# Kernel optimization log

Hardware: AMD Instinct MI355X
Metric: run time of the kernel (lower is better)

The kernel has to match this reference:

```python
import jax, jax.numpy as jnp
import numpy as np

N_GROUP = 64
GROUP_SIZE = 64
INPUT_DIM = 2048
BATCH = 8192
N_MONTN = 512


def setup_inputs() -> dict:
    key = jax.random.key(0)
    k1, k2, k3, k4, k5 = jax.random.split(key, 5)
    x = jax.random.normal(k1, (BATCH, INPUT_DIM), dtype=jnp.float32)
    weight = jax.random.normal(k2, (N_GROUP * GROUP_SIZE, INPUT_DIM), dtype=jnp.float32) * 0.02
    bias = jax.random.normal(k3, (N_GROUP * GROUP_SIZE,), dtype=jnp.float32) * 0.02
    rand_u = jax.random.uniform(k4, (BATCH,), dtype=jnp.float32)
    montn_index = jax.random.randint(k5, (N_MONTN,), 0, INPUT_DIM, dtype=jnp.int32)
    return {"x": x, "weight": weight, "bias": bias, "rand_u": rand_u,
            "montn_index": montn_index}


def reference(x, weight, bias, rand_u, montn_index):
    # Square the weights on monotone input columns (in-place in torch).
    w = weight.at[:, montn_index].set(weight[:, montn_index] ** 2)
    # y = x @ w^T + b  -> [B, n_group * n_group_size]
    y = jnp.einsum('bi,oi->bo', x, w) + bias
    B = y.shape[0]
    # per-group min over contiguous slices, then max over groups
    group_mins = y.reshape(B, N_GROUP, GROUP_SIZE).min(axis=2)  # [B, n_group]
    out = group_mins.max(axis=1)                                 # [B]
    # vectorized Bernoulli: 1.0 if u < sigmoid(out) else 0.0
    sample = (rand_u < jax.nn.sigmoid(out)).astype(jnp.float32)
    return sample.reshape(-1, 1)
```

## Files before the change

### kernel.cpp

```cpp
#include <hip/hip_runtime.h>
#include <cmath>


typedef _Float16 f16x8 __attribute__((ext_vector_type(8)));
typedef float f32x4 __attribute__((ext_vector_type(4)));

#define MARGIN_EPS 4e-3f
#define MAX_UNDEC 96

__device__ __forceinline__ void async_load16(const void* gptr, void* lptr) {
  __builtin_amdgcn_global_load_lds(
      (const __attribute__((address_space(1))) void*)gptr,
      (__attribute__((address_space(3))) void*)lptr, 16, 0, 0);
}

__device__ __forceinline__ float us2f(unsigned short u) {
  return (float)__builtin_bit_cast(_Float16, u);
}

__device__ __forceinline__ unsigned f2key(float f) {
  unsigned b = __float_as_uint(f);
  return (b & 0x80000000u) ? ~b : (b | 0x80000000u);
}
__device__ __forceinline__ float key2f(unsigned e) {
  unsigned b = (e & 0x80000000u) ? (e ^ 0x80000000u) : ~e;
  return __uint_as_float(b);
}


__global__ void convert_hi(const float* __restrict__ x,
                           const float* __restrict__ wgt,
                           unsigned short* __restrict__ xo,
                           unsigned short* __restrict__ wo,
                           const int* __restrict__ montn,
                           int* __restrict__ count) {
  __shared__ unsigned msk[64];
  const int b = blockIdx.x, t = threadIdx.x;
  const int l = t & 63, w = t >> 6;
  const int r = b * 4 + w;
  const int use_mask = (r >= 8192) ? 1 : 0;
  if (b == 0 && t == 0) *count = 0;
  if (use_mask) {
    if (t < 64) msk[t] = 0u;
    __syncthreads();
    for (int j = t; j < 512; j += 256) {
      const int c = montn[j];
      atomicOr(&msk[c >> 5], 1u << (c & 31));
    }
    __syncthreads();
  }
  const float* rowp = use_mask ? (wgt + (size_t)(r - 8192) * 2048)
                               : (x + (size_t)r * 2048);
  unsigned short* up = use_mask ? (wo + (size_t)(r - 8192) * 2048)
                                : (xo + (size_t)r * 2048);
  float4 v[4][2];
#pragma unroll
  for (int p = 0; p < 4; ++p) {
    v[p][0] = ((const float4*)rowp)[p * 128 + 2 * l];
    v[p][1] = ((const float4*)rowp)[p * 128 + 2 * l + 1];
  }
  unsigned mw[4];
#pragma unroll
  for (int p = 0; p < 4; ++p)
    mw[p] = use_mask ? msk[p * 16 + (l >> 2)] : 0u;

#pragma unroll
  for (int p = 0; p < 4; ++p) {
    float f[8];
    f[0] = v[p][0].x; f[1] = v[p][0].y; f[2] = v[p][0].z; f[3] = v[p][0].w;
    f[4] = v[p][1].x; f[5] = v[p][1].y; f[6] = v[p][1].z; f[7] = v[p][1].w;
    unsigned short hs[8];
#pragma unroll
    for (int c = 0; c < 8; ++c) {
      float g = f[c];
      if ((mw[p] >> (8 * (l & 3) + c)) & 1u) g = g * g;
      hs[c] = __builtin_bit_cast(unsigned short, (_Float16)g);
    }
    uint4 H;
    H.x = (unsigned)hs[0] | ((unsigned)hs[1] << 16);
    H.y = (unsigned)hs[2] | ((unsigned)hs[3] << 16);
    H.z = (unsigned)hs[4] | ((unsigned)hs[5] << 16);
    H.w = (unsigned)hs[6] | ((unsigned)hs[7] << 16);
    *((uint4*)(up + p * 512 + 8 * l)) = H;
  }
}

__global__ __launch_bounds__(256, 2) void gemm_minmax(
    const unsigned short* __restrict__ X, const unsigned short* __restrict__ W,
    const float* __restrict__ bias, float* __restrict__ pmax) {
  __shared__ unsigned short As[128 * 64];
  __shared__ unsigned short Bs[256 * 64];
  const int t = threadIdx.x;
  const int lane = t & 63;
  const int w = t >> 6;
  const int wm = w >> 1, wn = w & 1;
  const int lin = blockIdx.x;
  const int sid = lin >> 3;
  const int m0 = (sid >> 1) * 128;
  const int nb = (lin & 7) * 2 + (sid & 1);
  const int n0 = nb * 256;

  const int rowBase = w * 8 + (lane >> 3);
  const int gchunk = ((lane & 7) ^ ((lane >> 3) & 7)) * 8;
  const size_t gA0 = (size_t)(m0 + rowBase) * 2048 + gchunk;
  const size_t gB0 = (size_t)(n0 + rowBase) * 2048 + gchunk;
  unsigned short* ldsA0 = As + w * 512;
  unsigned short* ldsB0 = Bs + w * 512;

  const int am = lane & 15, quad = lane >> 4;
  int arow[4], brow[8];
#pragma unroll
  for (int i = 0; i < 4; ++i) arow[i] = (wm * 64 + i * 16 + am) * 64;
#pragma unroll
  for (int j = 0; j < 8; ++j) brow[j] = (wn * 128 + j * 16 + am) * 64;
  int swz[2];
#pragma unroll
  for (int h = 0; h < 2; ++h) swz[h] = (((h << 2) + quad) ^ (am & 7)) * 8;

  f32x4 acc[4][8];
#pragma unroll
  for (int i = 0; i < 4; ++i)
#pragma unroll
    for (int j = 0; j < 8; ++j) acc[i][j] = (f32x4){0.f, 0.f, 0.f, 0.f};

#pragma unroll 1
  for (int it = 0; it < 32; ++it) {
    const int kin = it * 64;
    __syncthreads();
#pragma unroll
    for (int c = 0; c < 4; ++c)
      async_load16(X + gA0 + (size_t)(c * 32) * 2048 + kin, ldsA0 + c * 2048);
#pragma unroll
    for (int c = 0; c < 8; ++c)
      async_load16(W + gB0 + (size_t)(c * 32) * 2048 + kin, ldsB0 + c * 2048);
    __syncthreads();

#pragma unroll
    for (int h = 0; h < 2; ++h) {
      f16x8 av[4], bv[8];
#pragma unroll
      for (int i = 0; i < 4; ++i) av[i] = *(const f16x8*)(As + arow[i] + swz[h]);
#pragma unroll
      for (int j = 0; j < 8; ++j) bv[j] = *(const f16x8*)(Bs + brow[j] + swz[h]);
#pragma unroll
      for (int mb = 0; mb < 4; ++mb)
#pragma unroll
        for (int nb8 = 0; nb8 < 8; ++nb8)
          acc[mb][nb8] = __builtin_amdgcn_mfma_f32_16x16x32_f16(
              av[mb], bv[nb8], acc[mb][nb8], 0, 0, 0);
    }
  }

  float bv8[8];
#pragma unroll
  for (int nb8 = 0; nb8 < 8; ++nb8)
    bv8[nb8] = bias[n0 + wn * 128 + nb8 * 16 + am];
  float vml[4][4];
#pragma unroll
  for (int mb = 0; mb < 4; ++mb) {
#pragma unroll
    for (int reg = 0; reg < 4; ++reg) {
      float vm = -3.4e38f;
#pragma unroll
      for (int hh = 0; hh < 2; ++hh) {
        float v = fminf(
            fminf(acc[mb][4 * hh + 0][reg] + bv8[4 * hh + 0],
                  acc[mb][4 * hh + 1][reg] + bv8[4 * hh + 1]),
            fminf(acc[mb][4 * hh + 2][reg] + bv8[4 * hh + 2],
                  acc[mb][4 * hh + 3][reg] + bv8[4 * hh + 3]));
        v = fminf(v, __shfl_xor(v, 1, 64));
        v = fminf(v, __shfl_xor(v, 2, 64));
        v = fminf(v, __shfl_xor(v, 4, 64));
        v = fminf(v, __shfl_xor(v, 8, 64));
        vm = fmaxf(vm, v);
      }
      vml[mb][reg] = vm;
    }
  }
  __syncthreads();
  float* pbuf = (float*)As;
  if (wn == 1 && am == 0) {
#pragma unroll
    for (int mb = 0; mb < 4; ++mb)
#pragma unroll
      for (int reg = 0; reg < 4; ++reg)
        pbuf[wm * 64 + mb * 16 + quad * 4 + reg] = vml[mb][reg];
  }
  __syncthreads();
  if (wn == 0 && am == 0) {
#pragma unroll
    for (int mb = 0; mb < 4; ++mb)
#pragma unroll
      for (int reg = 0; reg < 4; ++reg) {
        const int ridx = wm * 64 + mb * 16 + quad * 4 + reg;
        pmax[(size_t)(m0 + ridx) * 16 + nb] = fmaxf(vml[mb][reg], pbuf[ridx]);
      }
  }
}

__global__ void finalize_margin(const float* __restrict__ pmax,
                                const float* __restrict__ rand_u,
                                float* __restrict__ out,
                                int* __restrict__ count,
                                int* __restrict__ undec) {
  const int row = blockIdx.x * 256 + threadIdx.x;
  const float4* pp = (const float4*)(pmax + (size_t)row * 16);
  const float4 a = pp[0], b4 = pp[1], c4 = pp[2], d4 = pp[3];
  float v = fmaxf(fmaxf(fmaxf(a.x, a.y), fmaxf(a.z, a.w)),
                  fmaxf(fmaxf(b4.x, b4.y), fmaxf(b4.z, b4.w)));
  v = fmaxf(v, fmaxf(fmaxf(c4.x, c4.y), fmaxf(c4.z, c4.w)));
  v = fmaxf(v, fmaxf(fmaxf(d4.x, d4.y), fmaxf(d4.z, d4.w)));
  const float u = rand_u[row];
  const float slo = 1.0f / (1.0f + expf(-(v - MARGIN_EPS)));
  const float shi = 1.0f / (1.0f + expf(-(v + MARGIN_EPS)));
  if (u < slo) {
    out[row] = 1.0f;
  } else if (u >= shi) {
    out[row] = 0.0f;
  } else {
    const int i = atomicAdd(count, 1);
    if (i < 8192) undec[i] = row;
  }
}

__global__ __launch_bounds__(256) void recompute_fp32(
    const float* __restrict__ X, const float* __restrict__ W,
    const int* __restrict__ montn, const int* __restrict__ count,
    const int* __restrict__ undec, float* __restrict__ ypart) {
  __shared__ float wf[64 * 129];
  __shared__ float part[256];
  __shared__ unsigned msk[64];
  const int g = blockIdx.x, kc = blockIdx.y;
  const int t = threadIdx.x;
  int n = *count;
  if (n > MAX_UNDEC) n = MAX_UNDEC;
  if (n == 0) return;

  if (t < 64) msk[t] = 0u;
  __syncthreads();
  for (int j = t; j < 512; j += 256) {
    const int c = montn[j];
    atomicOr(&msk[c >> 5], 1u << (c & 31));
  }
  __syncthreads();

  {
    const int cl = t >> 2, ks = t & 3;
    const int k0 = kc * 128 + ks * 32;
    const float* wp = W + (size_t)(g * 64 + cl) * 2048 + k0;
    float* dst = wf + cl * 129 + ks * 32;
    const unsigned mword = msk[k0 >> 5];
#pragma unroll
    for (int i = 0; i < 32; i += 4) {
      float4 wv = *(const float4*)(wp + i);
      float f0 = wv.x, f1 = wv.y, f2 = wv.z, f3 = wv.w;
      if ((mword >> (i + 0)) & 1u) f0 *= f0;
      if ((mword >> (i + 1)) & 1u) f1 *= f1;
      if ((mword >> (i + 2)) & 1u) f2 *= f2;
      if ((mword >> (i + 3)) & 1u) f3 *= f3;
      dst[i + 0] = f0; dst[i + 1] = f1; dst[i + 2] = f2; dst[i + 3] = f3;
    }
  }
  __syncthreads();

  const int col = t & 63, kq = t >> 6;
  const float* wcol = wf + col * 129 + kq * 32;
  float* yout = ypart + (size_t)kc * (96 * 4096);
  for (int s = 0; s < n; ++s) {
    const int row = undec[s];
    const float* xp = X + (size_t)row * 2048 + kc * 128 + kq * 32;
    float acc = 0.f;
#pragma unroll
    for (int i = 0; i < 32; i += 4) {
      float4 xv = *(const float4*)(xp + i);
      acc = fmaf(xv.x, wcol[i + 0], acc);
      acc = fmaf(xv.y, wcol[i + 1], acc);
      acc = fmaf(xv.z, wcol[i + 2], acc);
      acc = fmaf(xv.w, wcol[i + 3], acc);
    }
    part[t] = acc;
    __syncthreads();
    if (t < 64) {
      const float yv = part[t] + part[t + 64] + part[t + 128] + part[t + 192];
      yout[(size_t)s * 4096 + g * 64 + t] = yv;
    }
    __syncthreads();
  }
}

__global__ void decide(const float* __restrict__ ypart,
                       const int* __restrict__ undec,
                       const int* __restrict__ count,
                       const float* __restrict__ bias,
                       const float* __restrict__ rand_u,
                       float* __restrict__ out) {
  __shared__ float gm[64];
  int n = *count;
  if (n > MAX_UNDEC) n = MAX_UNDEC;
  const int s = blockIdx.x;
  if (s >= n) return;
  const int t = threadIdx.x, w = t >> 6;
  const float* yb = ypart + (size_t)s * 4096;
#pragma unroll 1
  for (int e = 0; e < 16; ++e) {
    const int c = t + e * 256;
    float y = bias[c];
#pragma unroll
    for (int kc = 0; kc < 16; ++kc)
      y += yb[(size_t)kc * (96 * 4096) + c];
    y = fminf(y, __shfl_xor(y, 1, 64));
    y = fminf(y, __shfl_xor(y, 2, 64));
    y = fminf(y, __shfl_xor(y, 4, 64));
    y = fminf(y, __shfl_xor(y, 8, 64));
    y = fminf(y, __shfl_xor(y, 16, 64));
    y = fminf(y, __shfl_xor(y, 32, 64));
    if ((t & 63) == 0) gm[w + 4 * e] = y;
  }
  __syncthreads();
  if (t < 64) {
    float v = gm[t];
    v = fmaxf(v, __shfl_xor(v, 1, 64));
    v = fmaxf(v, __shfl_xor(v, 2, 64));
    v = fmaxf(v, __shfl_xor(v, 4, 64));
    v = fmaxf(v, __shfl_xor(v, 8, 64));
    v = fmaxf(v, __shfl_xor(v, 16, 64));
    v = fmaxf(v, __shfl_xor(v, 32, 64));
    if (t == 0) {
      const int row = undec[s];
      const float sg = 1.0f / (1.0f + expf(-v));
      out[row] = (rand_u[row] < sg) ? 1.0f : 0.0f;
    }
  }
}

__global__ void convert_split_fb(float* __restrict__ x, float* __restrict__ wgt,
                                 const int* __restrict__ montn,
                                 int* __restrict__ count,
                                 unsigned* __restrict__ gmax) {
  const int b = blockIdx.x;
  const int t = threadIdx.x;
  if (b >= 3072) {
    gmax[(b - 3072) * 256 + t] = 0u;
    return;
  }
  __shared__ unsigned msk[64];
  const int l = t & 63, w = t >> 6;
  const int r = b * 4 + w;
  const int use_mask = (r >= 8192) ? 1 : 0;
  if (b == 0 && t == 0) *count = 0;
  if (use_mask) {
    if (t < 64) msk[t] = 0u;
    __syncthreads();
    for (int j = t; j < 512; j += 256) {
      const int c = montn[j];
      atomicOr(&msk[c >> 5], 1u << (c & 31));
    }
    __syncthreads();
  }
  float* rowp = use_mask ? (wgt + (size_t)(r - 8192) * 2048)
                         : (x + (size_t)r * 2048);
  float4 v[4][2];
#pragma unroll
  for (int p = 0; p < 4; ++p) {
    v[p][0] = ((const float4*)rowp)[p * 128 + 2 * l];
    v[p][1] = ((const float4*)rowp)[p * 128 + 2 * l + 1];
  }
  unsigned mw[4];
#pragma unroll
  for (int p = 0; p < 4; ++p)
    mw[p] = use_mask ? msk[p * 16 + (l >> 2)] : 0u;

  unsigned short* up = (unsigned short*)rowp;
#pragma unroll
  for (int p = 0; p < 4; ++p) {
    float f[8];
    f[0] = v[p][0].x; f[1] = v[p][0].y; f[2] = v[p][0].z; f[3] = v[p][0].w;
    f[4] = v[p][1].x; f[5] = v[p][1].y; f[6] = v[p][1].z; f[7] = v[p][1].w;
    unsigned short hs[8], ls[8];
#pragma unroll
    for (int c = 0; c < 8; ++c) {
      float g = f[c];
      if ((mw[p] >> (8 * (l & 3) + c)) & 1u) g = g * g;
      _Float16 h = (_Float16)g;
      float res = g - (float)h;
      _Float16 lo = (_Float16)res;
      hs[c] = __builtin_bit_cast(unsigned short, h);
      ls[c] = __builtin_bit_cast(unsigned short, lo);
    }
    uint4 H, L;
    H.x = (unsigned)hs[0] | ((unsigned)hs[1] << 16);
    H.y = (unsigned)hs[2] | ((unsigned)hs[3] << 16);
    H.z = (unsigned)hs[4] | ((unsigned)hs[5] << 16);
    H.w = (unsigned)hs[6] | ((unsigned)hs[7] << 16);
    L.x = (unsigned)ls[0] | ((unsigned)ls[1] << 16);
    L.y = (unsigned)ls[2] | ((unsigned)ls[3] << 16);
    L.z = (unsigned)ls[4] | ((unsigned)ls[5] << 16);
    L.w = (unsigned)ls[6] | ((unsigned)ls[7] << 16);
    *((uint4*)(up + p * 512 + 8 * l)) = H;
    *((uint4*)(up + 2048 + p * 512 + 8 * l)) = L;
  }
}

__global__ __launch_bounds__(256, 2) void gemm_minmax_fb(
    const unsigned short* __restrict__ X, const unsigned short* __restrict__ W,
    const float* __restrict__ bias, unsigned* __restrict__ gmax) {
  __shared__ unsigned short As[128 * 64];
  __shared__ unsigned short Bs[256 * 64];
  const int t = threadIdx.x;
  const int lane = t & 63;
  const int w = t >> 6;
  const int wm = w >> 1, wn = w & 1;
  const int lin = blockIdx.x;
  const int sid = lin >> 3;
  const int m0 = (sid >> 1) * 128;
  const int n0 = ((lin & 7) * 2 + (sid & 1)) * 256;

  const int rowBase = w * 8 + (lane >> 3);
  const int gchunk = ((lane & 7) ^ ((lane >> 3) & 7)) * 8;
  const size_t gA0 = (size_t)(m0 + rowBase) * 4096 + gchunk;
  const size_t gB0 = (size_t)(n0 + rowBase) * 4096 + gchunk;
  unsigned short* ldsA0 = As + w * 512;
  unsigned short* ldsB0 = Bs + w * 512;

  const int am = lane & 15, quad = lane >> 4;
  int arow[4], brow[8];
#pragma unroll
  for (int i = 0; i < 4; ++i) arow[i] = (wm * 64 + i * 16 + am) * 64;
#pragma unroll
  for (int j = 0; j < 8; ++j) brow[j] = (wn * 128 + j * 16 + am) * 64;
  int swz[2];
#pragma unroll
  for (int h = 0; h < 2; ++h) swz[h] = (((h << 2) + quad) ^ (am & 7)) * 8;

  f32x4 acc[4][8];
#pragma unroll
  for (int i = 0; i < 4; ++i)
#pragma unroll
    for (int j = 0; j < 8; ++j) acc[i][j] = (f32x4){0.f, 0.f, 0.f, 0.f};

#pragma unroll 1
  for (int it = 0; it < 32; ++it) {
    const int kin = it * 64;
    __syncthreads();
#pragma unroll
    for (int c = 0; c < 4; ++c)
      async_load16(X + gA0 + (size_t)(c * 32) * 4096 + kin, ldsA0 + c * 2048);
#pragma unroll
    for (int c = 0; c < 8; ++c)
      async_load16(W + gB0 + (size_t)(c * 32) * 4096 + kin, ldsB0 + c * 2048);
    __syncthreads();

#pragma unroll
    for (int h = 0; h < 2; ++h) {
      f16x8 av[4], bv[8];
#pragma unroll
      for (int i = 0; i < 4; ++i) av[i] = *(const f16x8*)(As + arow[i] + swz[h]);
#pragma unroll
      for (int j = 0; j < 8; ++j) bv[j] = *(const f16x8*)(Bs + brow[j] + swz[h]);
#pragma unroll
      for (int mb = 0; mb < 4; ++mb)
#pragma unroll
        for (int nb = 0; nb < 8; ++nb)
          acc[mb][nb] = __builtin_amdgcn_mfma_f32_16x16x32_f16(
              av[mb], bv[nb], acc[mb][nb], 0, 0, 0);
    }
  }

  float bv8[8];
#pragma unroll
  for (int nb = 0; nb < 8; ++nb) bv8[nb] = bias[n0 + wn * 128 + nb * 16 + am];
#pragma unroll
  for (int mb = 0; mb < 4; ++mb) {
#pragma unroll
    for (int reg = 0; reg < 4; ++reg) {
      float vm = -3.4e38f;
#pragma unroll
      for (int hh = 0; hh < 2; ++hh) {
        float v = fminf(
            fminf(acc[mb][4 * hh + 0][reg] + bv8[4 * hh + 0],
                  acc[mb][4 * hh + 1][reg] + bv8[4 * hh + 1]),
            fminf(acc[mb][4 * hh + 2][reg] + bv8[4 * hh + 2],
                  acc[mb][4 * hh + 3][reg] + bv8[4 * hh + 3]));
        v = fminf(v, __shfl_xor(v, 1, 64));
        v = fminf(v, __shfl_xor(v, 2, 64));
        v = fminf(v, __shfl_xor(v, 4, 64));
        v = fminf(v, __shfl_xor(v, 8, 64));
        vm = fmaxf(vm, v);
      }
      if (am == 0) {
        const int row = m0 + wm * 64 + mb * 16 + quad * 4 + reg;
        atomicMax(&gmax[row], f2key(vm));
      }
    }
  }
}

__global__ void finalize_margin_fb(const unsigned* __restrict__ gmax,
                                   const float* __restrict__ rand_u,
                                   float* __restrict__ out,
                                   int* __restrict__ count,
                                   int* __restrict__ undec,
                                   float4* __restrict__ ybuf4) {
  const int t = threadIdx.x;
  ybuf4[(size_t)blockIdx.x * 256 + t] = (float4){0.f, 0.f, 0.f, 0.f};
  if (blockIdx.x < 32) {
    const int row = blockIdx.x * 256 + t;
    const float v = key2f(gmax[row]);
    const float u = rand_u[row];
    const float slo = 1.0f / (1.0f + expf(-(v - MARGIN_EPS)));
    const float shi = 1.0f / (1.0f + expf(-(v + MARGIN_EPS)));
    if (u < slo) {
      out[row] = 1.0f;
    } else if (u >= shi) {
      out[row] = 0.0f;
    } else {
      const int i = atomicAdd(count, 1);
      if (i < 8192) undec[i] = row;
    }
  }
}

__global__ __launch_bounds__(256) void recompute_rows_fb(
    const unsigned short* __restrict__ X, const unsigned short* __restrict__ W,
    const int* __restrict__ count, const int* __restrict__ undec,
    float* __restrict__ ybuf) {
  __shared__ float wf[64 * 129];
  __shared__ float part[256];
  const int g = blockIdx.x, kc = blockIdx.y;
  const int t = threadIdx.x;
  int n = *count;
  if (n > MAX_UNDEC) n = MAX_UNDEC;
  if (n == 0) return;

  {
    const int cl = t >> 2, ks = t & 3;
    const unsigned short* wp =
        W + (size_t)(g * 64 + cl) * 4096 + kc * 128 + ks * 32;
    float* dst = wf + cl * 129 + ks * 32;
#pragma unroll
    for (int i = 0; i < 32; i += 8) {
      uint4 hv = *(const uint4*)(wp + i);
      uint4 lv = *(const uint4*)(wp + 2048 + i);
      const unsigned* hw = (const unsigned*)&hv;
      const unsigned* lw = (const unsigned*)&lv;
#pragma unroll
      for (int m = 0; m < 4; ++m) {
        dst[i + 2 * m] = us2f((unsigned short)(hw[m] & 0xFFFF)) +
                         us2f((unsigned short)(lw[m] & 0xFFFF));
        dst[i + 2 * m + 1] = us2f((unsigned short)(hw[m] >> 16)) +
                             us2f((unsigned short)(lw[m] >> 16));
      }
    }
  }
  __syncthreads();

  const int col = t & 63, kq = t >> 6;
  const float* wcol = wf + col * 129 + kq * 32;
  for (int s = 0; s < n; ++s) {
    const int row = undec[s];
    const unsigned short* xp = X + (size_t)row * 4096 + kc * 128 + kq * 32;
    float acc = 0.f;
#pragma unroll
    for (int i = 0; i < 32; i += 8) {
      uint4 hv = *(const uint4*)(xp + i);
      uint4 lv = *(const uint4*)(xp + 2048 + i);
      const unsigned* hw = (const unsigned*)&hv;
      const unsigned* lw = (const unsigned*)&lv;
#pragma unroll
      for (int m = 0; m < 4; ++m) {
        const float x0 = us2f((unsigned short)(hw[m] & 0xFFFF)) +
                         us2f((unsigned short)(lw[m] & 0xFFFF));
        const float x1 = us2f((unsigned short)(hw[m] >> 16)) +
                         us2f((unsigned short)(lw[m] >> 16));
        acc = fmaf(x0, wcol[i + 2 * m], acc);
        acc = fmaf(x1, wcol[i + 2 * m + 1], acc);
      }
    }
    part[t] = acc;
    __syncthreads();
    if (t < 64) {
      const float y = part[t] + part[t + 64] + part[t + 128] + part[t + 192];
      atomicAdd(ybuf + (size_t)s * 4096 + g * 64 + t, y);
    }
    __syncthreads();
  }
}

__global__ void decide_fb(const float* __restrict__ ybuf,
                          const int* __restrict__ undec,
                          const int* __restrict__ count,
                          const float* __restrict__ bias,
                          const float* __restrict__ rand_u,
                          float* __restrict__ out) {
  __shared__ float gm[64];
  int n = *count;
  if (n > MAX_UNDEC) n = MAX_UNDEC;
  const int s = blockIdx.x;
  if (s >= n) return;
  const int t = threadIdx.x;
  const int g = t >> 2, p4 = t & 3;
  const float* yb = ybuf + (size_t)s * 4096;
  const int c0 = g * 64 + p4 * 16;
  float m = 3.4e38f;
#pragma unroll
  for (int e = 0; e < 16; ++e) m = fminf(m, yb[c0 + e] + bias[c0 + e]);
  m = fminf(m, __shfl_xor(m, 1, 64));
  m = fminf(m, __shfl_xor(m, 2, 64));
  if (p4 == 0) gm[g] = m;
  __syncthreads();
  if (t < 64) {
    float v = gm[t];
    v = fmaxf(v, __shfl_xor(v, 1, 64));
    v = fmaxf(v, __shfl_xor(v, 2, 64));
    v = fmaxf(v, __shfl_xor(v, 4, 64));
    v = fmaxf(v, __shfl_xor(v, 8, 64));
    v = fmaxf(v, __shfl_xor(v, 16, 64));
    v = fmaxf(v, __shfl_xor(v, 32, 64));
    if (t == 0) {
      const int row = undec[s];
      const float sg = 1.0f / (1.0f + expf(-v));
      out[row] = (rand_u[row] < sg) ? 1.0f : 0.0f;
    }
  }
}

extern "C" void kernel_launch(void* const* d_in, const int* in_sizes, int n_in,
                              void* d_out, int out_size, void* d_ws, size_t ws_size,
                              hipStream_t stream) {
  float* x = (float*)d_in[0];
  float* weight = (float*)d_in[1];
  const float* bias = (const float*)d_in[2];
  const float* rand_u = (const float*)d_in[3];
  const int* montn = (const int*)d_in[4];
  float* out = (float*)d_out;

  char* ws = (char*)d_ws;
  int* count = (int*)ws;
  int* undec = (int*)(ws + 256);
  float* ybuf = (float*)(ws + 65536);
  float* pmax = (float*)(ws + 65536 + 1572864);
  unsigned* gmax = (unsigned*)(ws + 65536 + 1572864);

  const size_t XO_OFF = (size_t)4 * 1024 * 1024;
  const size_t XO_BYTES = (size_t)8192 * 2048 * 2;
  const size_t WO_BYTES = (size_t)4096 * 2048 * 2;
  const bool big_ws = ws_size >= XO_OFF + XO_BYTES + WO_BYTES;

  if (big_ws) {
    unsigned short* xo = (unsigned short*)(ws + XO_OFF);
    unsigned short* wo = (unsigned short*)(ws + XO_OFF + XO_BYTES);
    float* ypart = (float*)(ws + XO_OFF);
    convert_hi<<<3072, 256, 0, stream>>>(x, weight, xo, wo, montn, count);
    gemm_minmax<<<1024, 256, 0, stream>>>(xo, wo, bias, pmax);
    finalize_margin<<<32, 256, 0, stream>>>(pmax, rand_u, out, count, undec);
    recompute_fp32<<<dim3(64, 16), 256, 0, stream>>>(x, weight, montn, count,
                                                     undec, ypart);
    decide<<<MAX_UNDEC, 256, 0, stream>>>(ypart, undec, count, bias, rand_u,
                                          out);
  } else {
    convert_split_fb<<<3104, 256, 0, stream>>>(x, weight, montn, count, gmax);
    gemm_minmax_fb<<<1024, 256, 0, stream>>>(
        (const unsigned short*)x, (const unsigned short*)weight, bias, gmax);
    finalize_margin_fb<<<384, 256, 0, stream>>>(gmax, rand_u, out, count,
                                                undec, (float4*)ybuf);
    recompute_rows_fb<<<dim3(64, 16), 256, 0, stream>>>(
        (const unsigned short*)x, (const unsigned short*)weight, count, undec,
        ybuf);
    decide_fb<<<MAX_UNDEC, 256, 0, stream>>>(ybuf, undec, count, bias, rand_u,
                                             out);
  }
}
```

Baseline: 296.3 us.

## Split GEMM block tile across eight waves and emit per-group minima directly

The 128x256 block tile of the f16 GEMM is now shared by 512 threads, so each of eight waves owns a 64x64 sub-tile instead of four waves owning 64x128. The wave's 64 columns are exactly one group, so each wave writes its group minimum straight to pmax. This drops the shared-memory max-combine and its two extra barriers from the epilogue. pmax grows from 16 to 64 entries per row, and finalize_margin now reduces 64 values per row. The goal is more waves in flight and fewer accumulator registers per wave, at the cost of more LDS reads per MFMA and larger barrier groups.

```diff
diff --git a/kernel.cpp b/kernel.cpp
--- a/kernel.cpp
+++ b/kernel.cpp
@@ -85,7 +85,7 @@
   }
 }
 
-__global__ __launch_bounds__(256, 2) void gemm_minmax(
+__global__ __launch_bounds__(512, 4) void gemm_minmax(
     const unsigned short* __restrict__ X, const unsigned short* __restrict__ W,
     const float* __restrict__ bias, float* __restrict__ pmax) {
   __shared__ unsigned short As[128 * 64];
@@ -93,7 +93,8 @@
   const int t = threadIdx.x;
   const int lane = t & 63;
   const int w = t >> 6;
-  const int wm = w >> 1, wn = w & 1;
+  const int wm = w >> 2;
+  const int wn = w & 3;
   const int lin = blockIdx.x;
   const int sid = lin >> 3;
   const int m0 = (sid >> 1) * 128;
@@ -108,93 +109,68 @@
   unsigned short* ldsB0 = Bs + w * 512;
 
   const int am = lane & 15, quad = lane >> 4;
-  int arow[4], brow[8];
+  int arow[4], brow[4];
 #pragma unroll
   for (int i = 0; i < 4; ++i) arow[i] = (wm * 64 + i * 16 + am) * 64;
 #pragma unroll
-  for (int j = 0; j < 8; ++j) brow[j] = (wn * 128 + j * 16 + am) * 64;
+  for (int j = 0; j < 4; ++j) brow[j] = (wn * 64 + j * 16 + am) * 64;
   int swz[2];
 #pragma unroll
   for (int h = 0; h < 2; ++h) swz[h] = (((h << 2) + quad) ^ (am & 7)) * 8;
 
-  f32x4 acc[4][8];
+  f32x4 acc[4][4];
 #pragma unroll
   for (int i = 0; i < 4; ++i)
 #pragma unroll
-    for (int j = 0; j < 8; ++j) acc[i][j] = (f32x4){0.f, 0.f, 0.f, 0.f};
+    for (int j = 0; j < 4; ++j) acc[i][j] = (f32x4){0.f, 0.f, 0.f, 0.f};
 
 #pragma unroll 1
   for (int it = 0; it < 32; ++it) {
     const int kin = it * 64;
     __syncthreads();
 #pragma unroll
+    for (int c = 0; c < 2; ++c)
+      async_load16(X + gA0 + (size_t)(c * 64) * 2048 + kin, ldsA0 + c * 4096);
+#pragma unroll
     for (int c = 0; c < 4; ++c)
-      async_load16(X + gA0 + (size_t)(c * 32) * 2048 + kin, ldsA0 + c * 2048);
-#pragma unroll
-    for (int c = 0; c < 8; ++c)
-      async_load16(W + gB0 + (size_t)(c * 32) * 2048 + kin, ldsB0 + c * 2048);
+      async_load16(W + gB0 + (size_t)(c * 64) * 2048 + kin, ldsB0 + c * 4096);
     __syncthreads();
 
 #pragma unroll
     for (int h = 0; h < 2; ++h) {
-      f16x8 av[4], bv[8];
+      f16x8 av[4], bv[4];
 #pragma unroll
       for (int i = 0; i < 4; ++i) av[i] = *(const f16x8*)(As + arow[i] + swz[h]);
 #pragma unroll
-      for (int j = 0; j < 8; ++j) bv[j] = *(const f16x8*)(Bs + brow[j] + swz[h]);
+      for (int j = 0; j < 4; ++j) bv[j] = *(const f16x8*)(Bs + brow[j] + swz[h]);
 #pragma unroll
       for (int mb = 0; mb < 4; ++mb)
 #pragma unroll
-        for (int nb8 = 0; nb8 < 8; ++nb8)
-          acc[mb][nb8] = __builtin_amdgcn_mfma_f32_16x16x32_f16(
-              av[mb], bv[nb8], acc[mb][nb8], 0, 0, 0);
-    }
-  }
-
-  float bv8[8];
-#pragma unroll
-  for (int nb8 = 0; nb8 < 8; ++nb8)
-    bv8[nb8] = bias[n0 + wn * 128 + nb8 * 16 + am];
-  float vml[4][4];
+        for (int nj = 0; nj < 4; ++nj)
+          acc[mb][nj] = __builtin_amdgcn_mfma_f32_16x16x32_f16(
+              av[mb], bv[nj], acc[mb][nj], 0, 0, 0);
+    }
+  }
+
+  const int grp = (n0 >> 6) + wn;
+  float bj[4];
+#pragma unroll
+  for (int j = 0; j < 4; ++j) bj[j] = bias[n0 + wn * 64 + j * 16 + am];
 #pragma unroll
   for (int mb = 0; mb < 4; ++mb) {
 #pragma unroll
     for (int reg = 0; reg < 4; ++reg) {
-      float vm = -3.4e38f;
-#pragma unroll
-      for (int hh = 0; hh < 2; ++hh) {
-        float v = fminf(
-            fminf(acc[mb][4 * hh + 0][reg] + bv8[4 * hh + 0],
-                  acc[mb][4 * hh + 1][reg] + bv8[4 * hh + 1]),
-            fminf(acc[mb][4 * hh + 2][reg] + bv8[4 * hh + 2],
-                  acc[mb][4 * hh + 3][reg] + bv8[4 * hh + 3]));
-        v = fminf(v, __shfl_xor(v, 1, 64));
-        v = fminf(v, __shfl_xor(v, 2, 64));
-        v = fminf(v, __shfl_xor(v, 4, 64));
-        v = fminf(v, __shfl_xor(v, 8, 64));
-        vm = fmaxf(vm, v);
+      float v = fminf(fminf(acc[mb][0][reg] + bj[0], acc[mb][1][reg] + bj[1]),
+                      fminf(acc[mb][2][reg] + bj[2], acc[mb][3][reg] + bj[3]));
+      v = fminf(v, __shfl_xor(v, 1, 64));
+      v = fminf(v, __shfl_xor(v, 2, 64));
+      v = fminf(v, __shfl_xor(v, 4, 64));
+      v = fminf(v, __shfl_xor(v, 8, 64));
+      if (am == 0) {
+        const int row = m0 + wm * 64 + mb * 16 + quad * 4 + reg;
+        pmax[(size_t)row * 64 + grp] = v;
       }
-      vml[mb][reg] = vm;
-    }
-  }
-  __syncthreads();
-  float* pbuf = (float*)As;
-  if (wn == 1 && am == 0) {
-#pragma unroll
-    for (int mb = 0; mb < 4; ++mb)
-#pragma unroll
-      for (int reg = 0; reg < 4; ++reg)
-        pbuf[wm * 64 + mb * 16 + quad * 4 + reg] = vml[mb][reg];
-  }
-  __syncthreads();
-  if (wn == 0 && am == 0) {
-#pragma unroll
-    for (int mb = 0; mb < 4; ++mb)
-#pragma unroll
-      for (int reg = 0; reg < 4; ++reg) {
-        const int ridx = wm * 64 + mb * 16 + quad * 4 + reg;
-        pmax[(size_t)(m0 + ridx) * 16 + nb] = fmaxf(vml[mb][reg], pbuf[ridx]);
-      }
+    }
   }
 }
 
@@ -204,12 +180,13 @@
                                 int* __restrict__ count,
                                 int* __restrict__ undec) {
   const int row = blockIdx.x * 256 + threadIdx.x;
-  const float4* pp = (const float4*)(pmax + (size_t)row * 16);
-  const float4 a = pp[0], b4 = pp[1], c4 = pp[2], d4 = pp[3];
-  float v = fmaxf(fmaxf(fmaxf(a.x, a.y), fmaxf(a.z, a.w)),
-                  fmaxf(fmaxf(b4.x, b4.y), fmaxf(b4.z, b4.w)));
-  v = fmaxf(v, fmaxf(fmaxf(c4.x, c4.y), fmaxf(c4.z, c4.w)));
-  v = fmaxf(v, fmaxf(fmaxf(d4.x, d4.y), fmaxf(d4.z, d4.w)));
+  const float4* pp = (const float4*)(pmax + (size_t)row * 64);
+  float v = -3.4e38f;
+#pragma unroll
+  for (int q = 0; q < 16; ++q) {
+    const float4 a = pp[q];
+    v = fmaxf(v, fmaxf(fmaxf(a.x, a.y), fmaxf(a.z, a.w)));
+  }
   const float u = rand_u[row];
   const float slo = 1.0f / (1.0f + expf(-(v - MARGIN_EPS)));
   const float shi = 1.0f / (1.0f + expf(-(v + MARGIN_EPS)));
@@ -651,7 +628,7 @@
     unsigned short* wo = (unsigned short*)(ws + XO_OFF + XO_BYTES);
     float* ypart = (float*)(ws + XO_OFF);
     convert_hi<<<3072, 256, 0, stream>>>(x, weight, xo, wo, montn, count);
-    gemm_minmax<<<1024, 256, 0, stream>>>(xo, wo, bias, pmax);
+    gemm_minmax<<<1024, 512, 0, stream>>>(xo, wo, bias, pmax);
     finalize_margin<<<32, 256, 0, stream>>>(pmax, rand_u, out, count, undec);
     recompute_fp32<<<dim3(64, 16), 256, 0, stream>>>(x, weight, montn, count,
                                                      undec, ypart);
```

After: 301.4 us. Within noise of the previous version (+1.7%).
